# Optimization experiments

Measured on AMD Instinct MI355X. Metric: run time of the kernel, lower is better.

Reference implementation:

```python
import jax, jax.numpy as jnp
import numpy as np

BATCH = 2      # batch_size (number of videos)
NUM_HEADS = 8


def setup_inputs() -> dict:
    key = jax.random.key(0)
    k1, k2, k3 = jax.random.split(key, 3)
    B, H, W, C = 16, 64, 64, 512
    return {
        "hidden_states": jax.random.normal(k1, (B, H, W, C), dtype=jnp.float32),
        "w_qkv": jax.random.normal(k2, (3 * C, C), dtype=jnp.float32) * (C ** -0.5),
        "b_qkv": jax.random.normal(k3, (3 * C,), dtype=jnp.float32) * 0.02,
    }


def reference(hidden_states, w_qkv, b_qkv):
    B, H, W, C = hidden_states.shape
    bs, nh = BATCH, NUM_HEADS
    f = B // bs                      # video_length
    hd = C // nh                     # head_dim
    scale = hd ** -0.5

    # qkv projection (torch Linear: x @ W.T + b)
    qkv = hidden_states @ w_qkv.T + b_qkv                       # [B,H,W,3C]
    qkv = qkv.reshape(B, H * W, 3, nh, hd)
    qkv = qkv.transpose(2, 0, 3, 1, 4).reshape(3, B * nh, H * W, hd)
    q, k, v = qkv[0], qkv[1], qkv[2]                            # [B*nh, HW, hd]

    # NOTE: original rearrange labels '(b n f)' but memory layout is (b f) n;
    # it is a pure reshape, so replicate as flat reshape (faithful to math).
    q = q.reshape(bs, nh, f, H, W, hd)
    k = k.reshape(bs, nh, f, H, W, hd)
    v = v.reshape(bs, nh, f, H, W, hd)

    # q cat is identity; k/v: prepend last frame == cyclic roll by +1 on frames
    k = jnp.roll(k, 1, axis=2)
    v = jnp.roll(v, 1, axis=2)

    q = q.reshape(bs, nh, f, H * W, hd)
    # faithful flat reshape (scrambles (h,w,c) -> (hd, HW) order, as in torch)
    k = k.reshape(bs, nh, f, hd, H * W)
    v = v.reshape(bs, nh, f, H * W, hd)

    # einsums with NO contracted index: elementwise-transpose products
    attn = jnp.einsum('bnfhw,bnfwh->bnhfw', q * scale, k)       # [bs,nh,HW,f,hd]
    attn = jax.nn.softmax(attn, axis=-1)
    x = jnp.einsum('bnhfw,bnfhw->bnhfw', attn, v)               # [bs,nh,HW,f,hd]

    # faithful flat reshape (torch .view on contiguous tensor)
    x = x.reshape(bs, nh, f, H, W, hd)
    # rearrange 'b n f h w c -> (b f) h w (n c)'
    x = x.transpose(0, 2, 3, 4, 1, 5).reshape(bs * f, H, W, nh * hd)
    return x
```

## Files before the change

### kernel.cpp

```cpp
#include <hip/hip_runtime.h>
#include <math.h>


typedef _Float16 half8 __attribute__((ext_vector_type(8)));
typedef _Float16 half4 __attribute__((ext_vector_type(4)));
typedef __fp16 fp16x2 __attribute__((ext_vector_type(2)));
typedef float f32x4 __attribute__((ext_vector_type(4)));

__device__ __forceinline__ half8 pk8(const float4 x, const float4 y) {
    fp16x2 a = __builtin_amdgcn_cvt_pkrtz(x.x, x.y);
    fp16x2 b = __builtin_amdgcn_cvt_pkrtz(x.z, x.w);
    fp16x2 c = __builtin_amdgcn_cvt_pkrtz(y.x, y.y);
    fp16x2 d = __builtin_amdgcn_cvt_pkrtz(y.z, y.w);
    half8 r;
    r[0] = (_Float16)a[0]; r[1] = (_Float16)a[1];
    r[2] = (_Float16)b[0]; r[3] = (_Float16)b[1];
    r[4] = (_Float16)c[0]; r[5] = (_Float16)c[1];
    r[6] = (_Float16)d[0]; r[7] = (_Float16)d[1];
    return r;
}

__device__ __forceinline__ void gload_lds16(const void* g, void* l) {
    __builtin_amdgcn_global_load_lds(
        (const __attribute__((address_space(1))) unsigned int*)g,
        (__attribute__((address_space(3))) unsigned int*)l, 16, 0, 0);
}

__global__ __launch_bounds__(256) void cvt_fp16(
    const float* __restrict__ src, _Float16* __restrict__ dst)
{
    const size_t i = (size_t)blockIdx.x * 256 + threadIdx.x;
    const float4 x = *reinterpret_cast<const float4*>(src + i * 8);
    const float4 y = *reinterpret_cast<const float4*>(src + i * 8 + 4);
    *reinterpret_cast<half8*>(dst + i * 8) = pk8(x, y);
}

__global__ __launch_bounds__(256) void cvt_w_frag(
    const float* __restrict__ W, _Float16* __restrict__ Wf)
{
    const int gid  = blockIdx.x * 256 + threadIdx.x;
    const int lane = gid & 63;
    const int nf   = (gid >> 6) & 3;
    const int ks   = (gid >> 8) & 15;
    const int ntw  = gid >> 12;
    const float* src =
        W + (size_t)(ntw * 64 + nf * 16 + (lane & 15)) * 512 +
        ks * 32 + (lane >> 4) * 8;
    const float4 x = *reinterpret_cast<const float4*>(src);
    const float4 y = *reinterpret_cast<const float4*>(src + 4);
    *reinterpret_cast<half8*>(Wf + (size_t)gid * 8) = pk8(x, y);
}

__global__ __launch_bounds__(256, 4) void gemm_qkv_wf(
    const _Float16* __restrict__ Ah, const _Float16* __restrict__ Wf,
    const float* __restrict__ bias, _Float16* __restrict__ C)
{
    __shared__ __align__(16) _Float16 lds[12288];

    const int lin = blockIdx.x;
    const int swz = (lin & 7) * 768 + (lin >> 3);
    const int nt = swz % 12, mt = swz / 12;
    const int row0 = mt * 128, col0 = nt * 128;

    const int tid = threadIdx.x, wid = tid >> 6, lane = tid & 63;
    const int wm = wid >> 1, wn = wid & 1, l15 = lane & 15, kq = lane >> 4;

    const int s0  = wid * 2;
    const int rA0 = s0 * 16 + (lane >> 2);
    const int rA1 = rA0 + 16;
    const int c0  = (lane & 3) ^ ((rA0 >> 1) & 3);
    const int c1  = (lane & 3) ^ ((rA1 >> 1) & 3);
    const _Float16* ga0 = Ah + (size_t)(row0 + rA0) * 512 + c0 * 8;
    const _Float16* ga1 = Ah + (size_t)(row0 + rA1) * 512 + c1 * 8;

    const _Float16* wfb = Wf + (size_t)(nt * 2 + wn) * 32768 + lane * 8;

    f32x4 acc[4][4];
#pragma unroll
    for (int i = 0; i < 4; ++i)
#pragma unroll
        for (int j = 0; j < 4; ++j) acc[i][j] = (f32x4)0.f;

    half8 wfa[4], wfb_[4];

#define STAGE_A(KB, BUF)                                                       \
    do {                                                                       \
        _Float16* bdst = lds + (BUF) * 4096;                                   \
        gload_lds16(ga0 + (KB), bdst + s0 * 512);                              \
        gload_lds16(ga1 + (KB), bdst + (s0 + 1) * 512);                        \
    } while (0)

#define LOAD_W(DST, KS)                                                        \
    do {                                                                       \
        _Pragma("unroll")                                                      \
        for (int nf = 0; nf < 4; ++nf)                                         \
            DST[nf] = *reinterpret_cast<const half8*>(                         \
                wfb + (KS) * 2048 + nf * 512);                                 \
    } while (0)

#define FRAG_MFMA(BC, WU)                                                      \
    do {                                                                       \
        half8 ah[4];                                                           \
        _Pragma("unroll")                                                      \
        for (int mf = 0; mf < 4; ++mf) {                                       \
            const int r  = wm * 64 + mf * 16 + l15;                            \
            const int ph = (kq ^ ((r >> 1) & 3)) * 8;                          \
            ah[mf] = *reinterpret_cast<const half8*>((BC) + r * 32 + ph);      \
        }                                                                      \
        __builtin_amdgcn_s_setprio(1);                                         \
        _Pragma("unroll")                                                      \
        for (int nf = 0; nf < 4; ++nf)                                         \
            _Pragma("unroll")                                                  \
            for (int mf = 0; mf < 4; ++mf)                                     \
                acc[mf][nf] = __builtin_amdgcn_mfma_f32_16x16x32_f16(          \
                    ah[mf], WU[nf], acc[mf][nf], 0, 0, 0);                     \
        __builtin_amdgcn_s_setprio(0);                                         \
    } while (0)

#define STEP(T, WU, WL)                                                        \
    do {                                                                       \
        const int t2 = ((T) + 2 < 16) ? (T) + 2 : 15;                          \
        const int t1 = ((T) + 1 < 16) ? (T) + 1 : 15;                          \
        int sb = cb + 2; if (sb >= 3) sb -= 3;                                 \
        STAGE_A(t2 * 32, sb);                                                  \
        __builtin_amdgcn_sched_barrier(0);     \
        LOAD_W(WL, t1);                                                        \
        FRAG_MFMA(lds + cb * 4096, WU);                                        \
        __builtin_amdgcn_sched_barrier(0);                                     \
        __builtin_amdgcn_s_barrier();                                          \
        __builtin_amdgcn_sched_barrier(0);                                     \
        cb = (cb == 2) ? 0 : cb + 1;                                           \
    } while (0)

    STAGE_A(0, 0);
    STAGE_A(32, 1);
    __builtin_amdgcn_sched_barrier(0);
    LOAD_W(wfa, 0);
    asm volatile("s_waitcnt vmcnt(4)" ::: "memory");
    __builtin_amdgcn_sched_barrier(0);
    __builtin_amdgcn_s_barrier();
    __builtin_amdgcn_sched_barrier(0);

    int cb = 0;
#pragma unroll 1
    for (int t = 0; t < 16; t += 2) {
        STEP(t,     wfa, wfb_);
        STEP(t + 1, wfb_, wfa);
    }
#undef STEP
#undef FRAG_MFMA
#undef LOAD_W
#undef STAGE_A

    float* wbase = reinterpret_cast<float*>(lds) + wid * 1088;
    const float4 bv4 = *reinterpret_cast<const float4*>(
        &bias[col0 + wn * 64 + l15 * 4]);

#pragma unroll
    for (int mf = 0; mf < 4; ++mf) {
#pragma unroll
        for (int nf = 0; nf < 4; ++nf)
#pragma unroll
            for (int j = 0; j < 4; ++j)
                wbase[(kq * 4 + j) * 68 + nf * 16 + l15] = acc[mf][nf][j];
        __syncthreads();
#pragma unroll
        for (int i = 0; i < 4; ++i) {
            const int r16 = i * 4 + kq;
            float4 v = *reinterpret_cast<float4*>(wbase + r16 * 68 + l15 * 4);
            half4 h;
            h[0] = (_Float16)(v.x + bv4.x);
            h[1] = (_Float16)(v.y + bv4.y);
            h[2] = (_Float16)(v.z + bv4.z);
            h[3] = (_Float16)(v.w + bv4.w);
            const int r = row0 + wm * 64 + mf * 16 + r16;
            *reinterpret_cast<half4*>(
                &C[(size_t)r * 1536 + col0 + wn * 64 + l15 * 4]) = h;
        }
        __syncthreads();
    }
}

__global__ __launch_bounds__(256) void attn_scramble(
    const _Float16* __restrict__ qkv, float* __restrict__ out)
{
    __shared__ float Ks[64][68];
    const int bid = blockIdx.x;
    const int hw6 = bid & 63;
    const int n   = (bid >> 6) & 7;
    const int b   = bid >> 9;
    const int kn  = (n + 7) & 7;
    const int t   = threadIdx.x;
    {
        const int lx = t & 7;
        const int rp = t >> 3;
#pragma unroll
        for (int p = 0; p < 2; ++p) {
            const int dp = p * 32 + rp;
            const half8 kv = *reinterpret_cast<const half8*>(
                &qkv[(size_t)(b * 4096 + dp * 64 + hw6) * 1536 + 512 +
                     kn * 64 + lx * 8]);
#pragma unroll
            for (int e = 0; e < 8; ++e)
                Ks[lx * 8 + e][dp] = (float)kv[e];
        }
    }
    __syncthreads();
    const int row = t >> 2;
    const int tl  = t & 3;
    const size_t rbase = (size_t)(b * 4096 + hw6 * 64 + row) * 1536;
    float s[16];
    {
        const _Float16* qp = qkv + rbase + n * 64 + tl * 16;
        const half8 q0 = *reinterpret_cast<const half8*>(qp);
        const half8 q1 = *reinterpret_cast<const half8*>(qp + 8);
        float q[16], kk[16];
#pragma unroll
        for (int e = 0; e < 8; ++e) {
            q[e] = (float)q0[e];
            q[8 + e] = (float)q1[e];
        }
#pragma unroll
        for (int u = 0; u < 4; ++u)
            *reinterpret_cast<float4*>(&kk[u * 4]) =
                *reinterpret_cast<const float4*>(&Ks[row][tl * 16 + u * 4]);
        float m = -1e30f;
#pragma unroll
        for (int u = 0; u < 16; ++u) {
            s[u] = 0.125f * q[u] * kk[u];
            m = fmaxf(m, s[u]);
        }
        m = fmaxf(m, __shfl_xor(m, 1));
        m = fmaxf(m, __shfl_xor(m, 2));
        float sum = 0.f;
#pragma unroll
        for (int u = 0; u < 16; ++u) {
            s[u] = __expf(s[u] - m);
            sum += s[u];
        }
        sum += __shfl_xor(sum, 1);
        sum += __shfl_xor(sum, 2);
        const float inv = 1.0f / sum;
#pragma unroll
        for (int u = 0; u < 16; ++u) s[u] *= inv;
    }
    const _Float16* vp = qkv + rbase + 1024 + kn * 64 + tl * 16;
    const half8 v0 = *reinterpret_cast<const half8*>(vp);
    const half8 v1 = *reinterpret_cast<const half8*>(vp + 8);
    const int vb = b >> 3, fr = b & 7;
    float* op = out +
        ((size_t)(((vb * 8 + (hw6 >> 3)) * 64 + ((hw6 & 7) * 8 + (row >> 3))) * 64 +
                  ((row & 7) * 8 + n)) * 512) + fr * 64 + tl * 16;
    float4 o0, o1, o2, o3;
    o0.x = s[0]  * (float)v0[0]; o0.y = s[1]  * (float)v0[1];
    o0.z = s[2]  * (float)v0[2]; o0.w = s[3]  * (float)v0[3];
    o1.x = s[4]  * (float)v0[4]; o1.y = s[5]  * (float)v0[5];
    o1.z = s[6]  * (float)v0[6]; o1.w = s[7]  * (float)v0[7];
    o2.x = s[8]  * (float)v1[0]; o2.y = s[9]  * (float)v1[1];
    o2.z = s[10] * (float)v1[2]; o2.w = s[11] * (float)v1[3];
    o3.x = s[12] * (float)v1[4]; o3.y = s[13] * (float)v1[5];
    o3.z = s[14] * (float)v1[6]; o3.w = s[15] * (float)v1[7];
    *reinterpret_cast<float4*>(op)      = o0;
    *reinterpret_cast<float4*>(op + 4)  = o1;
    *reinterpret_cast<float4*>(op + 8)  = o2;
    *reinterpret_cast<float4*>(op + 12) = o3;
}

extern "C" void kernel_launch(void* const* d_in, const int* in_sizes, int n_in,
                              void* d_out, int out_size, void* d_ws, size_t ws_size,
                              hipStream_t stream) {
    const float* hs = (const float*)d_in[0];
    const float* w  = (const float*)d_in[1];
    const float* bq = (const float*)d_in[2];
    float* out = (float*)d_out;
    _Float16* qkv = (_Float16*)d_ws;

    _Float16* Asp = (_Float16*)d_out;
    _Float16* Wf  = Asp + 33554432;

    cvt_fp16<<<16384, 256, 0, stream>>>(hs, Asp);
    cvt_w_frag<<<384, 256, 0, stream>>>(w, Wf);
    gemm_qkv_wf<<<6144, 256, 0, stream>>>(Asp, Wf, bq, qkv);
    attn_scramble<<<8192, 256, 0, stream>>>(qkv, out);
}
```

Measured before the change: 233.1 us.

## Fuse fp32-to-fp16 activation conversion into the QKV GEMM A-tile staging

Removes the separate cvt_fp16 pass over hidden_states. The GEMM now loads fp32 A tiles straight into registers, packs them to fp16 and writes them to LDS, replacing the direct global-to-LDS async loads. A register prefetch one step further ahead keeps global latency overlapped. This saves a full read and write of the 128 MB activation tensor, but each GEMM tile now reads fp32 A (twice the bytes) across the 12 N-tiles and needs more registers and VALU work.

```diff
diff --git a/kernel.cpp b/kernel.cpp
--- a/kernel.cpp
+++ b/kernel.cpp
@@ -18,21 +18,6 @@
     r[4] = (_Float16)c[0]; r[5] = (_Float16)c[1];
     r[6] = (_Float16)d[0]; r[7] = (_Float16)d[1];
     return r;
-}
-
-__device__ __forceinline__ void gload_lds16(const void* g, void* l) {
-    __builtin_amdgcn_global_load_lds(
-        (const __attribute__((address_space(1))) unsigned int*)g,
-        (__attribute__((address_space(3))) unsigned int*)l, 16, 0, 0);
-}
-
-__global__ __launch_bounds__(256) void cvt_fp16(
-    const float* __restrict__ src, _Float16* __restrict__ dst)
-{
-    const size_t i = (size_t)blockIdx.x * 256 + threadIdx.x;
-    const float4 x = *reinterpret_cast<const float4*>(src + i * 8);
-    const float4 y = *reinterpret_cast<const float4*>(src + i * 8 + 4);
-    *reinterpret_cast<half8*>(dst + i * 8) = pk8(x, y);
 }
 
 __global__ __launch_bounds__(256) void cvt_w_frag(
@@ -51,8 +36,8 @@
     *reinterpret_cast<half8*>(Wf + (size_t)gid * 8) = pk8(x, y);
 }
 
-__global__ __launch_bounds__(256, 4) void gemm_qkv_wf(
-    const _Float16* __restrict__ Ah, const _Float16* __restrict__ Wf,
+__global__ __launch_bounds__(256, 4) void gemm_qkv_fuse(
+    const float* __restrict__ A, const _Float16* __restrict__ Wf,
     const float* __restrict__ bias, _Float16* __restrict__ C)
 {
     __shared__ __align__(16) _Float16 lds[12288];
@@ -70,8 +55,8 @@
     const int rA1 = rA0 + 16;
     const int c0  = (lane & 3) ^ ((rA0 >> 1) & 3);
     const int c1  = (lane & 3) ^ ((rA1 >> 1) & 3);
-    const _Float16* ga0 = Ah + (size_t)(row0 + rA0) * 512 + c0 * 8;
-    const _Float16* ga1 = Ah + (size_t)(row0 + rA1) * 512 + c1 * 8;
+    const float* ga0 = A + (size_t)(row0 + rA0) * 512 + c0 * 8;
+    const float* ga1 = A + (size_t)(row0 + rA1) * 512 + c1 * 8;
 
     const _Float16* wfb = Wf + (size_t)(nt * 2 + wn) * 32768 + lane * 8;
 
@@ -82,12 +67,21 @@
         for (int j = 0; j < 4; ++j) acc[i][j] = (f32x4)0.f;
 
     half8 wfa[4], wfb_[4];
-
-#define STAGE_A(KB, BUF)                                                       \
-    do {                                                                       \
-        _Float16* bdst = lds + (BUF) * 4096;                                   \
-        gload_lds16(ga0 + (KB), bdst + s0 * 512);                              \
-        gload_lds16(ga1 + (KB), bdst + (s0 + 1) * 512);                        \
+    float4 pa0, pa1, pb0, pb1;
+
+#define LOAD_A(KB)                                                             \
+    do {                                                                       \
+        pa0 = *reinterpret_cast<const float4*>(ga0 + (KB));                    \
+        pa1 = *reinterpret_cast<const float4*>(ga0 + (KB) + 4);                \
+        pb0 = *reinterpret_cast<const float4*>(ga1 + (KB));                    \
+        pb1 = *reinterpret_cast<const float4*>(ga1 + (KB) + 4);                \
+    } while (0)
+
+#define WRITE_A(BUF)                                                           \
+    do {                                                                       \
+        _Float16* bd = lds + (BUF) * 4096;                                     \
+        *reinterpret_cast<half8*>(bd + s0 * 512 + lane * 8)       = pk8(pa0, pa1);\
+        *reinterpret_cast<half8*>(bd + (s0 + 1) * 512 + lane * 8) = pk8(pb0, pb1);\
     } while (0)
 
 #define LOAD_W(DST, KS)                                                        \
@@ -119,24 +113,27 @@
 
 #define STEP(T, WU, WL)                                                        \
     do {                                                                       \
-        const int t2 = ((T) + 2 < 16) ? (T) + 2 : 15;                          \
-        const int t1 = ((T) + 1 < 16) ? (T) + 1 : 15;                          \
+        const int t1  = ((T) + 1 < 16) ? (T) + 1 : 15;                         \
+        const int kb3 = (((T) + 3 < 16) ? (T) + 3 : 15) * 32;                  \
         int sb = cb + 2; if (sb >= 3) sb -= 3;                                 \
-        STAGE_A(t2 * 32, sb);                                                  \
-        __builtin_amdgcn_sched_barrier(0);     \
+        WRITE_A(sb);                                                           \
+        LOAD_A(kb3);                                                           \
         LOAD_W(WL, t1);                                                        \
         FRAG_MFMA(lds + cb * 4096, WU);                                        \
+        asm volatile("s_waitcnt lgkmcnt(0)" ::: "memory");                     \
         __builtin_amdgcn_sched_barrier(0);                                     \
         __builtin_amdgcn_s_barrier();                                          \
         __builtin_amdgcn_sched_barrier(0);                                     \
         cb = (cb == 2) ? 0 : cb + 1;                                           \
     } while (0)
 
-    STAGE_A(0, 0);
-    STAGE_A(32, 1);
-    __builtin_amdgcn_sched_barrier(0);
+    LOAD_A(0);
+    WRITE_A(0);
+    LOAD_A(32);
+    WRITE_A(1);
+    LOAD_A(64);
     LOAD_W(wfa, 0);
-    asm volatile("s_waitcnt vmcnt(4)" ::: "memory");
+    asm volatile("s_waitcnt lgkmcnt(0)" ::: "memory");
     __builtin_amdgcn_sched_barrier(0);
     __builtin_amdgcn_s_barrier();
     __builtin_amdgcn_sched_barrier(0);
@@ -150,7 +147,8 @@
 #undef STEP
 #undef FRAG_MFMA
 #undef LOAD_W
-#undef STAGE_A
+#undef WRITE_A
+#undef LOAD_A
 
     float* wbase = reinterpret_cast<float*>(lds) + wid * 1088;
     const float4 bv4 = *reinterpret_cast<const float4*>(
@@ -275,11 +273,9 @@
     float* out = (float*)d_out;
     _Float16* qkv = (_Float16*)d_ws;
 
-    _Float16* Asp = (_Float16*)d_out;
-    _Float16* Wf  = Asp + 33554432;
-
-    cvt_fp16<<<16384, 256, 0, stream>>>(hs, Asp);
+    _Float16* Wf = (_Float16*)d_out;
+
     cvt_w_frag<<<384, 256, 0, stream>>>(w, Wf);
-    gemm_qkv_wf<<<6144, 256, 0, stream>>>(Asp, Wf, bq, qkv);
+    gemm_qkv_fuse<<<6144, 256, 0, stream>>>(hs, Wf, bq, qkv);
     attn_scramble<<<8192, 256, 0, stream>>>(qkv, out);
 }
```

Result: slower. 803.9 us (+244.9%).
